# Performance work log

Measured on AMD Instinct MI355X. Metric: run time of the kernel, lower is better.

Reference implementation:

```python
import jax, jax.numpy as jnp
import numpy as np

X_DIM, XC_DIM, G_DIM = 45, 10, 20
P_DIM = XC_DIM * G_DIM  # 200
N_ITER, KAPPA, LAMDA, YITA = 5, 0.8, 0.9999, 0.5
B = 131072


def _mlp(h, W1, b1, W2, b2):
    # MLP(in,out) with activation=(elu, None): elu hidden, linear out
    return jax.nn.elu(h @ W1 + b1) @ W2 + b2


def _f_p(h):
    # hippocampal nonlinearity: leaky_relu clamped to [-1, 1]
    return jnp.clip(jax.nn.leaky_relu(h), -1.0, 1.0)


def _retrieve(q, M0):
    # iterative Hopfield-like attractor retrieval (n_iteration fixed, small)
    p = q
    for _ in range(N_ITER):
        p = _f_p(KAPPA * p + p @ M0)
    return p


def setup_inputs() -> dict:
    key = jax.random.key(0)
    ks = jax.random.split(key, 12)
    s = 0.1  # small param scale for numerical sanity
    return {
        "x": jax.random.normal(ks[0], (B, X_DIM), jnp.float32),
        "g": jax.random.normal(ks[1], (B, G_DIM), jnp.float32),
        # M buffer starts at zeros in the module; use small noise so retrieval is nontrivial
        "M": 0.01 * jax.random.normal(ks[2], (1, P_DIM, P_DIM), jnp.float32),
        "W_comp": s * jax.random.normal(ks[3], (X_DIM, XC_DIM), jnp.float32),
        "W1_ie": s * jax.random.normal(ks[4], (G_DIM, 2 * G_DIM), jnp.float32),
        "b1_ie": jnp.zeros((2 * G_DIM,), jnp.float32),
        "W2_ie": s * jax.random.normal(ks[5], (2 * G_DIM, G_DIM), jnp.float32),
        "b2_ie": jnp.zeros((G_DIM,), jnp.float32),
        "W1_gg": s * jax.random.normal(ks[6], (G_DIM, 2 * G_DIM), jnp.float32),
        "b1_gg": jnp.zeros((2 * G_DIM,), jnp.float32),
        "W2_gg": s * jax.random.normal(ks[7], (2 * G_DIM, G_DIM), jnp.float32),
        "b2_gg": jnp.zeros((G_DIM,), jnp.float32),
        "W_sp": s * jax.random.normal(ks[8], (XC_DIM, X_DIM), jnp.float32),
        "b_sp": jnp.zeros((X_DIM,), jnp.float32),
    }


def reference(x, g, M, W_comp, W1_ie, b1_ie, W2_ie, b2_ie,
              W1_gg, b1_gg, W2_gg, b2_gg, W_sp, b_sp):
    # fixed structural matrices (buffers in torch)
    W_tile = jnp.kron(jnp.ones((1, G_DIM), jnp.float32), jnp.eye(XC_DIM, dtype=jnp.float32))   # [xc, p]
    W_repeat = jnp.kron(jnp.eye(G_DIM, dtype=jnp.float32), jnp.ones((1, XC_DIM), jnp.float32))  # [g, p]
    M0 = M[0]

    # compress sensory -> hippocampal sensory component
    xc = x @ W_comp                 # [B, xc]
    x_ = xc @ W_tile                # [B, p]

    # retrieve from memory with sensory cue, infer entorhinal g
    px = _retrieve(x_, M0)          # [B, p]
    g_inf = jnp.clip(_mlp(px @ W_repeat.T, W1_ie, b1_ie, W2_ie, b2_ie), -1.0, 1.0)  # [B, g]

    # path integration / entorhinal transition, project to hippocampus
    g2 = jnp.tanh(_mlp(g, W1_gg, b1_gg, W2_gg, b2_gg))  # [B, g]
    g_ = g2 @ W_repeat              # [B, p]

    # retrieve with entorhinal cue, predict sensory observation
    p = _retrieve(g_, M0)           # [B, p]
    x_inf = (p @ W_tile.T) @ W_sp + b_sp  # [B, x]

    # inferred hippocampal state (conjunction) and Hebbian memory update
    p_inf = _f_p(g_ * x_)           # [B, p]
    hebb = ((p_inf - p).T @ (p_inf + p)) / jnp.asarray(x.shape[0], x.dtype)  # [p, p]
    M_new = LAMDA * M + YITA * hebb[None]

    return (g_inf, x_inf, g_, x_, M_new)
```

## Files before the change

### kernel.cpp

```cpp
#include <hip/hip_runtime.h>

#define B_TOTAL 131072
#define PD 200
#define KAPPA 0.8f
#define LAMDA 0.9999f
#define YITA 0.5f
#define MS_KS 216
#define HB_RS 72

typedef short short8 __attribute__((ext_vector_type(8)));
typedef short short4v __attribute__((ext_vector_type(4)));
typedef float f32x16 __attribute__((ext_vector_type(16)));
typedef unsigned uint4v __attribute__((ext_vector_type(4)));

static __device__ __forceinline__ float bf2f(unsigned short h) {
  union { unsigned u; float f; } v; v.u = ((unsigned)h) << 16; return v.f;
}
static __device__ __forceinline__ unsigned short f2bf(float f) {
  union { float f; unsigned u; } v; v.f = f;
  unsigned r = v.u + 0x7FFFu + ((v.u >> 16) & 1u);
  return (unsigned short)(r >> 16);
}
static __device__ __forceinline__ float fp_nl(float v) {
  float t = fmaxf(v, 0.01f * v);
  return fminf(1.f, fmaxf(-1.f, t));
}
static __device__ __forceinline__ unsigned pkbf(float lo, float hi) {
  unsigned r;
  asm("v_cvt_pk_bf16_f32 %0, %1, %2" : "=v"(r) : "v"(lo), "v"(hi));
  return r;
}
static __device__ __forceinline__ void swap32(unsigned &a, unsigned &b) {
  asm("s_nop 1\n\tv_permlane32_swap_b32 %0, %1" : "+v"(a), "+v"(b));
}
static __device__ __forceinline__ uint4v mk4(unsigned a, unsigned b, unsigned c, unsigned d) {
  uint4v v; v[0] = a; v[1] = b; v[2] = c; v[3] = d; return v;
}
static __device__ __forceinline__ short8 u4s8(uint4v w) {
  union { uint4v u; short8 s; } x; x.u = w; return x.s;
}

__global__ void tem_init_m(const float* __restrict__ Min, float* __restrict__ oM) {
  int i = blockIdx.x * 256 + threadIdx.x;
  if (i < PD * PD) oM[i] = LAMDA * Min[i];
}

__global__ __launch_bounds__(256, 4) void tem_pre(
    const float* __restrict__ xin, const float* __restrict__ gin,
    const float* __restrict__ Wc,
    const float* __restrict__ W1gg, const float* __restrict__ b1gg,
    const float* __restrict__ W2gg, const float* __restrict__ b2gg,
    float* __restrict__ o_g, float* __restrict__ o_x) {
  __shared__ unsigned short xcS[128 * 10];
  __shared__ float g2S[128 * 20];
  const int tid = threadIdx.x;
  const int r0 = blockIdx.x * 128;

  if (tid < 128) {
    const int rq = r0 + tid;
    float gv[20];
#pragma unroll
    for (int i = 0; i < 20; ++i) gv[i] = gin[(size_t)rq * 20 + i];
    float out20[20];
#pragma unroll
    for (int o = 0; o < 20; ++o) out20[o] = b2gg[o];
#pragma unroll 1
    for (int u = 0; u < 40; ++u) {
      float hu = b1gg[u];
#pragma unroll
      for (int i = 0; i < 20; ++i) hu += gv[i] * W1gg[i * 40 + u];
      hu = (hu > 0.f) ? hu : (expf(hu) - 1.f);
#pragma unroll
      for (int o = 0; o < 20; ++o) out20[o] += hu * W2gg[u * 20 + o];
    }
#pragma unroll
    for (int o = 0; o < 20; ++o) g2S[tid * 20 + o] = tanhf(out20[o]);
  } else {
    const int rr2 = tid - 128;
    const int rq = r0 + rr2;
    float xc[10];
#pragma unroll
    for (int o = 0; o < 10; ++o) xc[o] = 0.f;
#pragma unroll 1
    for (int j = 0; j < 45; ++j) {
      const float xv = xin[(size_t)rq * 45 + j];
#pragma unroll
      for (int o = 0; o < 10; ++o) xc[o] += xv * Wc[j * 10 + o];
    }
#pragma unroll
    for (int o = 0; o < 10; ++o) xcS[rr2 * 10 + o] = f2bf(xc[o]);
  }
  __syncthreads();
  for (int i = tid; i < 128 * 200; i += 256) {
    const int rP = i / 200, j = i - rP * 200;
    o_g[(size_t)(r0 + rP) * 200 + j] = g2S[rP * 20 + j / 10];
    o_x[(size_t)(r0 + rP) * 200 + j] = bf2f(xcS[rP * 10 + (j % 10)]);
  }
}

#define LDMS(nt, kc) (*(const short8*)(Ms + (((nt) * 32 + cl) * MS_KS + (kc) * 16 + hi * 8)))
#define MFMA_AG(ACC, A, B) asm("v_mfma_f32_32x32x16_bf16 %0, %1, %2, %0" : "+a"(ACC) : "v"(A), "v"(B))

#define STEP(PF, KC) do { \
  const short8 _b = u4s8(PF); \
  { const short8 _a = LDMS(0, KC); MFMA_AG(acc0, _a, _b); } \
  { const short8 _a = LDMS(1, KC); MFMA_AG(acc1, _a, _b); } \
  { const short8 _a = LDMS(2, KC); MFMA_AG(acc2, _a, _b); } \
  { const short8 _a = LDMS(3, KC); MFMA_AG(acc3, _a, _b); } \
  { const short8 _a = LDMS(4, KC); MFMA_AG(acc4, _a, _b); } \
  { const short8 _a = LDMS(5, KC); MFMA_AG(acc5, _a, _b); } \
  { const short8 _a = LDMS(6, KC); MFMA_AG(acc6, _a, _b); } \
  __builtin_amdgcn_sched_barrier(0); \
} while (0)

#define REPACK_LO(ACC, PF) do { \
  unsigned P0 = pkbf(fp_nl(ACC[0]), fp_nl(ACC[1])); \
  unsigned P1 = pkbf(fp_nl(ACC[2]), fp_nl(ACC[3])); \
  unsigned P2 = pkbf(fp_nl(ACC[4]), fp_nl(ACC[5])); \
  unsigned P3 = pkbf(fp_nl(ACC[6]), fp_nl(ACC[7])); \
  swap32(P0, P2); swap32(P1, P3); \
  PF = mk4(P0, P1, P2, P3); \
} while (0)
#define REPACK_HI(ACC, PF) do { \
  unsigned P4 = pkbf(fp_nl(ACC[8]),  fp_nl(ACC[9])); \
  unsigned P5 = pkbf(fp_nl(ACC[10]), fp_nl(ACC[11])); \
  unsigned P6 = pkbf(fp_nl(ACC[12]), fp_nl(ACC[13])); \
  unsigned P7 = pkbf(fp_nl(ACC[14]), fp_nl(ACC[15])); \
  swap32(P4, P6); swap32(P5, P7); \
  PF = mk4(P4, P5, P6, P7); \
} while (0)

#define ITER5 do { \
  f32x16 acc0 = {}, acc1 = {}, acc2 = {}, acc3 = {}, acc4 = {}, acc5 = {}, acc6 = {}; \
  STEP(pfA0, 0);  STEP(pfA1, 1);  STEP(pfA2, 2);  STEP(pfA3, 3); \
  STEP(pfA4, 4);  STEP(pfA5, 5);  STEP(pfA6, 6);  STEP(pfA7, 7); \
  STEP(pfA8, 8);  STEP(pfA9, 9);  STEP(pfA10, 10); STEP(pfA11, 11); \
  STEP(pfA12, 12); \
  REPACK_LO(acc0, pfA0);  REPACK_HI(acc0, pfA1); \
  REPACK_LO(acc1, pfA2);  REPACK_HI(acc1, pfA3); \
  REPACK_LO(acc2, pfA4);  REPACK_HI(acc2, pfA5); \
  REPACK_LO(acc3, pfA6);  REPACK_HI(acc3, pfA7); \
  REPACK_LO(acc4, pfA8);  REPACK_HI(acc4, pfA9); \
  REPACK_LO(acc5, pfA10); REPACK_HI(acc5, pfA11); \
  REPACK_LO(acc6, pfA12); \
} while (0)

#define FORR_LO(M_) M_(pfA0,0) M_(pfA1,16) M_(pfA2,32) M_(pfA3,48) M_(pfA4,64) M_(pfA5,80) \
                    M_(pfA6,96) M_(pfA7,112) M_(pfA8,128) M_(pfA9,144) M_(pfA10,160) M_(pfA11,176) M_(pfA12,192)
#define FORR_HI(M_) M_(pfA0,8) M_(pfA1,24) M_(pfA2,40) M_(pfA3,56) M_(pfA4,72) M_(pfA5,88) \
                    M_(pfA6,104) M_(pfA7,120) M_(pfA8,136) M_(pfA9,152) M_(pfA10,168) M_(pfA11,184)

#define INX(PF, BB) PF = mk4( \
  pkbf(xcv[((BB) + 0) % 10], xcv[((BB) + 1) % 10]), \
  pkbf(xcv[((BB) + 2) % 10], xcv[((BB) + 3) % 10]), \
  pkbf(xcv[((BB) + 4) % 10], xcv[((BB) + 5) % 10]), \
  pkbf(xcv[((BB) + 6) % 10], xcv[((BB) + 7) % 10]));
#define ING(PF, BB) PF = mk4( \
  pkbf(g2v[((BB) + 0) / 10], g2v[((BB) + 1) / 10]), \
  pkbf(g2v[((BB) + 2) / 10], g2v[((BB) + 3) / 10]), \
  pkbf(g2v[((BB) + 4) / 10], g2v[((BB) + 5) / 10]), \
  pkbf(g2v[((BB) + 6) / 10], g2v[((BB) + 7) / 10]));

#define E1W(W, F) { bins[(F) / 10] += bf2f((unsigned short)((W) & 0xFFFFu)); \
                    bins[((F) + 1) / 10] += bf2f((unsigned short)((W) >> 16)); }
#define E1PF(PF, BB) { E1W(PF[0], (BB) + 0) E1W(PF[1], (BB) + 2) E1W(PF[2], (BB) + 4) E1W(PF[3], (BB) + 6) }

#define E2AW(W, F) { ta[(F) % 10] += bf2f((unsigned short)((W) & 0xFFFFu)); \
                     ta[((F) + 1) % 10] += bf2f((unsigned short)((W) >> 16)); }
#define E2APF(PF, BB) { E2AW(PF[0], (BB) + 0) E2AW(PF[1], (BB) + 2) E2AW(PF[2], (BB) + 4) E2AW(PF[3], (BB) + 6) }

#define STG(PF, SL) (((uint4v*)Stg)[(wid * 4 + (SL)) * 64 + lane] = PF)

__global__ __launch_bounds__(512, 1) void tem_main(
    const float* __restrict__ xin, const float* __restrict__ gin,
    const float* __restrict__ Min, const float* __restrict__ Wc,
    const float* __restrict__ W1ie, const float* __restrict__ b1ie,
    const float* __restrict__ W2ie, const float* __restrict__ b2ie,
    const float* __restrict__ W1gg, const float* __restrict__ b1gg,
    const float* __restrict__ W2gg, const float* __restrict__ b2gg,
    const float* __restrict__ Wsp, const float* __restrict__ bsp,
    float* __restrict__ o_ginf, float* __restrict__ o_xinf,
    unsigned short* __restrict__ dWp, unsigned short* __restrict__ sWp) {
  __shared__ __attribute__((aligned(16))) unsigned short Ms[224 * MS_KS];
  __shared__ unsigned short xcS[256 * 10];
  __shared__ float g2S[256 * 20];
  __shared__ __attribute__((aligned(16))) unsigned Stg[8 * 4 * 64 * 4];

  const int tid = threadIdx.x;
  const int lane = tid & 63;
  const int wid = tid >> 6;
  const int cl = lane & 31;
  const int hi = lane >> 5;
  const int r0 = blockIdx.x * 256;

  {
    unsigned* Ms32 = (unsigned*)Ms;
    for (int i = tid; i < 224 * MS_KS / 2; i += 512) Ms32[i] = 0u;
  }
  __syncthreads();
  for (int i = tid; i < 200 * 224; i += 512) {
    const int k = i / 224, n = i - k * 224;
    if (n < 200) {
      float v = Min[k * 200 + n];
      if (k == n) v += KAPPA;
      Ms[n * MS_KS + k] = f2bf(v);
    }
  }

  if (tid < 256) {
    const int rq = r0 + tid;
    float gv[20];
#pragma unroll
    for (int i = 0; i < 20; ++i) gv[i] = gin[(size_t)rq * 20 + i];
    float h[40];
#pragma unroll
    for (int u = 0; u < 40; ++u) h[u] = b1gg[u];
#pragma unroll
    for (int i = 0; i < 20; ++i)
#pragma unroll
      for (int u = 0; u < 40; ++u) h[u] += gv[i] * W1gg[i * 40 + u];
#pragma unroll
    for (int u = 0; u < 40; ++u) h[u] = (h[u] > 0.f) ? h[u] : (expf(h[u]) - 1.f);
#pragma unroll
    for (int o = 0; o < 20; ++o) {
      float v = b2gg[o];
#pragma unroll
      for (int u = 0; u < 40; ++u) v += h[u] * W2gg[u * 20 + o];
      g2S[tid * 20 + o] = tanhf(v);
    }
  } else {
    const int rr2 = tid - 256;
    const int rq = r0 + rr2;
    float xc[10];
#pragma unroll
    for (int o = 0; o < 10; ++o) xc[o] = 0.f;
#pragma unroll 1
    for (int j = 0; j < 45; ++j) {
      const float xv = xin[(size_t)rq * 45 + j];
#pragma unroll
      for (int o = 0; o < 10; ++o) xc[o] += xv * Wc[j * 10 + o];
    }
#pragma unroll
    for (int o = 0; o < 10; ++o) xcS[rr2 * 10 + o] = f2bf(xc[o]);
  }
  __syncthreads();

  const int rr = wid * 32 + cl;
  const int r = r0 + rr;

  uint4v pfA0, pfA1, pfA2, pfA3, pfA4, pfA5, pfA6, pfA7, pfA8, pfA9, pfA10, pfA11, pfA12;

  {
    float xcv[10];
#pragma unroll
    for (int o = 0; o < 10; ++o) xcv[o] = bf2f(xcS[rr * 10 + o]);
    if (hi == 0) { FORR_LO(INX) }
    else         { FORR_HI(INX) pfA12 = mk4(0u, 0u, 0u, 0u); }
  }
#pragma unroll 1
  for (int it = 0; it < 5; ++it) { ITER5; }
  {
    float bins[20];
#pragma unroll
    for (int t = 0; t < 20; ++t) bins[t] = 0.f;
    if (hi == 0) { FORR_LO(E1PF) } else { FORR_HI(E1PF) }
#pragma unroll
    for (int t = 0; t < 20; ++t) bins[t] += __shfl_xor(bins[t], 32);
    float h[40];
#pragma unroll
    for (int u = 0; u < 40; ++u) h[u] = b1ie[u];
#pragma unroll
    for (int gg = 0; gg < 20; ++gg) {
      const float bv = bins[gg];
#pragma unroll
      for (int u = 0; u < 40; ++u) h[u] += bv * W1ie[gg * 40 + u];
    }
#pragma unroll
    for (int u = 0; u < 40; ++u) h[u] = (h[u] > 0.f) ? h[u] : (expf(h[u]) - 1.f);
#pragma unroll
    for (int oi = 0; oi < 10; ++oi) {
      const int o = hi * 10 + oi;
      float v = b2ie[o];
#pragma unroll
      for (int u = 0; u < 40; ++u) v += h[u] * W2ie[u * 20 + o];
      o_ginf[(size_t)r * 20 + o] = fminf(1.f, fmaxf(-1.f, v));
    }
  }

  {
    float g2v[20];
#pragma unroll
    for (int o = 0; o < 20; ++o) g2v[o] = g2S[rr * 20 + o];
    if (hi == 0) { FORR_LO(ING) }
    else         { FORR_HI(ING) pfA12 = mk4(0u, 0u, 0u, 0u); }
  }
#pragma unroll 1
  for (int it = 0; it < 5; ++it) { ITER5; }
  {
    float ta[10];
#pragma unroll
    for (int t = 0; t < 10; ++t) ta[t] = 0.f;
    if (hi == 0) { FORR_LO(E2APF) } else { FORR_HI(E2APF) }
#pragma unroll
    for (int t = 0; t < 10; ++t) ta[t] += __shfl_xor(ta[t], 32);
    const int o0 = hi ? 23 : 0, o1 = hi ? 45 : 23;
#pragma unroll 1
    for (int o = o0; o < o1; ++o) {
      float v = bsp[o];
#pragma unroll
      for (int a = 0; a < 10; ++a) v += ta[a] * Wsp[a * 45 + o];
      o_xinf[(size_t)r * 45 + o] = v;
    }
  }
  {
    unsigned int* dW32 = (unsigned int*)dWp;
    unsigned int* sW32 = (unsigned int*)sWp;
#pragma unroll 1
    for (int rnd = 0; rnd < 4; ++rnd) {
      if (rnd == 0)      { STG(pfA0, 0);  STG(pfA1, 1);  STG(pfA2, 2);   STG(pfA3, 3);  }
      else if (rnd == 1) { STG(pfA4, 0);  STG(pfA5, 1);  STG(pfA6, 2);   STG(pfA7, 3);  }
      else if (rnd == 2) { STG(pfA8, 0);  STG(pfA9, 1);  STG(pfA10, 2);  STG(pfA11, 3); }
      else               { STG(pfA12, 0); }
      asm volatile("s_waitcnt lgkmcnt(0)" ::: "memory");
      __builtin_amdgcn_sched_barrier(0);
      const int nIt = (rnd == 3) ? 2 : 16;
#pragma unroll 1
      for (int itw = 0; itw < nIt; ++itw) {
        const int idx = itw * 64 + lane;
        const int row = idx >> 5;
        const int jpo = idx & 31;
        const int jp = rnd * 32 + jpo;
        if (jp < 100) {
          const int kcl = jpo >> 3, rem = jpo & 7;
          const int hi2 = rem >> 2, jw = rem & 3;
          const unsigned word = Stg[(((wid * 4 + kcl) * 2 + hi2) * 32 + row) * 4 + jw];
          const int rB = wid * 32 + row;
          const int j0 = jp * 2;
          const float p0 = bf2f((unsigned short)(word & 0xFFFFu));
          const float p1 = bf2f((unsigned short)(word >> 16));
          const float x0 = bf2f(xcS[rB * 10 + (j0 % 10)]);
          const float x1 = bf2f(xcS[rB * 10 + ((j0 + 1) % 10)]);
          const float pi0 = fp_nl(g2S[rB * 20 + (j0 / 10)] * x0);
          const float pi1 = fp_nl(g2S[rB * 20 + ((j0 + 1) / 10)] * x1);
          const unsigned dpack = (unsigned)f2bf(pi0 - p0) | ((unsigned)f2bf(pi1 - p1) << 16);
          const unsigned spack = (unsigned)f2bf(pi0 + p0) | ((unsigned)f2bf(pi1 + p1) << 16);
          const size_t oidx = (size_t)(r0 + rB) * 100 + jp;
          dW32[oidx] = dpack;
          sW32[oidx] = spack;
        }
      }
      __builtin_amdgcn_sched_barrier(0);
    }
  }
}

__global__ __launch_bounds__(448, 1) void tem_hebb(
    const unsigned short* __restrict__ dWp, const unsigned short* __restrict__ sWp,
    float* __restrict__ oM) {
  __shared__ __attribute__((aligned(16))) unsigned short dT[224 * HB_RS];
  __shared__ __attribute__((aligned(16))) unsigned short sT[224 * HB_RS];
  const int tid = threadIdx.x;
  const int lane = tid & 63, wid = tid >> 6;
  const int cl = lane & 31, hi = lane >> 5;
  for (int i = tid; i < 224 * HB_RS; i += 448) { dT[i] = 0; sT[i] = 0; }
  f32x16 hacc[7];
#pragma unroll
  for (int nt = 0; nt < 7; ++nt)
#pragma unroll
    for (int q = 0; q < 16; ++q) hacc[nt][q] = 0.f;
  const int kbase = blockIdx.x * 512;
#pragma unroll 1
  for (int sub = 0; sub < 8; ++sub) {
    __syncthreads();
    const int kb = kbase + sub * 64;
#pragma unroll 1
    for (int i = tid; i < 64 * 50; i += 448) {
      const int rr = i / 50, fq = i - rr * 50;
      const int f0 = fq * 4;
      const short4v d4 = *(const short4v*)(dWp + ((size_t)(kb + rr) * 200 + f0));
      const short4v s4 = *(const short4v*)(sWp + ((size_t)(kb + rr) * 200 + f0));
#pragma unroll
      for (int q = 0; q < 4; ++q) {
        dT[(f0 + q) * HB_RS + rr] = (unsigned short)d4[q];
        sT[(f0 + q) * HB_RS + rr] = (unsigned short)s4[q];
      }
    }
    __syncthreads();
#pragma unroll
    for (int kc = 0; kc < 4; ++kc) {
      const short8 af = *(const short8*)(dT + ((wid * 32 + cl) * HB_RS + kc * 16 + hi * 8));
#pragma unroll
      for (int nt = 0; nt < 7; ++nt) {
        const short8 bfr = *(const short8*)(sT + ((nt * 32 + cl) * HB_RS + kc * 16 + hi * 8));
        hacc[nt] = __builtin_amdgcn_mfma_f32_32x32x16_bf16(af, bfr, hacc[nt], 0, 0, 0);
      }
    }
  }
  const float scale = YITA / (float)B_TOTAL;
#pragma unroll
  for (int nt = 0; nt < 7; ++nt) {
    const int j = nt * 32 + cl;
    if (j < 200) {
#pragma unroll
      for (int rg = 0; rg < 16; ++rg) {
        const int ii = wid * 32 + (rg & 3) + 8 * (rg >> 2) + 4 * hi;
        if (ii < 200) atomicAdd(&oM[ii * 200 + j], hacc[nt][rg] * scale);
      }
    }
  }
}

extern "C" void kernel_launch(void* const* d_in, const int* in_sizes, int n_in,
                              void* d_out, int out_size, void* d_ws, size_t ws_size,
                              hipStream_t stream) {
  (void)in_sizes; (void)n_in; (void)out_size; (void)ws_size;
  const float* xin  = (const float*)d_in[0];
  const float* gin  = (const float*)d_in[1];
  const float* Min  = (const float*)d_in[2];
  const float* Wc   = (const float*)d_in[3];
  const float* W1ie = (const float*)d_in[4];
  const float* b1ie = (const float*)d_in[5];
  const float* W2ie = (const float*)d_in[6];
  const float* b2ie = (const float*)d_in[7];
  const float* W1gg = (const float*)d_in[8];
  const float* b1gg = (const float*)d_in[9];
  const float* W2gg = (const float*)d_in[10];
  const float* b2gg = (const float*)d_in[11];
  const float* Wsp  = (const float*)d_in[12];
  const float* bsp  = (const float*)d_in[13];

  float* out = (float*)d_out;
  float* o_ginf = out;
  float* o_xinf = out + (size_t)B_TOTAL * 20;
  float* o_g    = out + (size_t)B_TOTAL * 65;
  float* o_x    = out + (size_t)B_TOTAL * 265;
  float* o_M    = out + (size_t)B_TOTAL * 465;

  unsigned short* dWp = (unsigned short*)d_ws;
  unsigned short* sWp = dWp + (size_t)B_TOTAL * PD;

  tem_init_m<<<(PD * PD + 255) / 256, 256, 0, stream>>>(Min, o_M);
  tem_pre<<<1024, 256, 0, stream>>>(xin, gin, Wc, W1gg, b1gg, W2gg, b2gg, o_g, o_x);
  tem_main<<<512, 512, 0, stream>>>(xin, gin, Min, Wc, W1ie, b1ie, W2ie, b2ie,
                                    W1gg, b1gg, W2gg, b2gg, Wsp, bsp,
                                    o_ginf, o_xinf, dWp, sWp);
  tem_hebb<<<256, 448, 0, stream>>>(dWp, sWp, o_M);
}
```

Measured before the change: 495.2 us.

## Store Hebbian workspace feature-major and stage per-row outputs through LDS

The d/s workspace is now written feature-major ([200][B]) rather than row-major, so the Hebbian kernel can load MFMA fragments straight from global memory without the LDS transpose and its two barriers per sub-chunk. The g_inf and x_inf outputs are also staged in shared memory and written back coalesced rather than as strided per-row stores. The trade-offs are extra block-wide syncs in the main kernel, only 2 of 8 waves writing the workspace, and unstaged global loads in the Hebbian kernel that reuse the A fragment less.

```diff
diff --git a/kernel.cpp b/kernel.cpp
--- a/kernel.cpp
+++ b/kernel.cpp
@@ -6,10 +6,8 @@
 #define LAMDA 0.9999f
 #define YITA 0.5f
 #define MS_KS 216
-#define HB_RS 72
 
 typedef short short8 __attribute__((ext_vector_type(8)));
-typedef short short4v __attribute__((ext_vector_type(4)));
 typedef float f32x16 __attribute__((ext_vector_type(16)));
 typedef unsigned uint4v __attribute__((ext_vector_type(4)));
 
@@ -169,7 +167,7 @@
                      ta[((F) + 1) % 10] += bf2f((unsigned short)((W) >> 16)); }
 #define E2APF(PF, BB) { E2AW(PF[0], (BB) + 0) E2AW(PF[1], (BB) + 2) E2AW(PF[2], (BB) + 4) E2AW(PF[3], (BB) + 6) }
 
-#define STG(PF, SL) (((uint4v*)Stg)[(wid * 4 + (SL)) * 64 + lane] = PF)
+#define STG(PF, SL) (((uint4v*)StgRaw)[(wid * 4 + (SL)) * 64 + lane] = PF)
 
 __global__ __launch_bounds__(512, 1) void tem_main(
     const float* __restrict__ xin, const float* __restrict__ gin,
@@ -184,7 +182,10 @@
   __shared__ __attribute__((aligned(16))) unsigned short Ms[224 * MS_KS];
   __shared__ unsigned short xcS[256 * 10];
   __shared__ float g2S[256 * 20];
-  __shared__ __attribute__((aligned(16))) unsigned Stg[8 * 4 * 64 * 4];
+  __shared__ __attribute__((aligned(16))) char StgRaw[32768];
+
+  unsigned* StgU = (unsigned*)StgRaw;
+  float* StgF = (float*)StgRaw;
 
   const int tid = threadIdx.x;
   const int lane = tid & 63;
@@ -283,9 +284,12 @@
       float v = b2ie[o];
 #pragma unroll
       for (int u = 0; u < 40; ++u) v += h[u] * W2ie[u * 20 + o];
-      o_ginf[(size_t)r * 20 + o] = fminf(1.f, fmaxf(-1.f, v));
-    }
-  }
+      StgF[rr * 20 + o] = fminf(1.f, fmaxf(-1.f, v));
+    }
+  }
+  __syncthreads();
+  for (int i = tid; i < 256 * 20; i += 512) o_ginf[(size_t)r0 * 20 + i] = StgF[i];
+  __syncthreads();
 
   {
     float g2v[20];
@@ -303,13 +307,23 @@
     if (hi == 0) { FORR_LO(E2APF) } else { FORR_HI(E2APF) }
 #pragma unroll
     for (int t = 0; t < 10; ++t) ta[t] += __shfl_xor(ta[t], 32);
-    const int o0 = hi ? 23 : 0, o1 = hi ? 45 : 23;
-#pragma unroll 1
-    for (int o = o0; o < o1; ++o) {
-      float v = bsp[o];
-#pragma unroll
-      for (int a = 0; a < 10; ++a) v += ta[a] * Wsp[a * 45 + o];
-      o_xinf[(size_t)r * 45 + o] = v;
+#pragma unroll 1
+    for (int ph = 0; ph < 2; ++ph) {
+      if ((rr >> 7) == ph) {
+        const int rL = rr & 127;
+        const int o0 = hi ? 23 : 0, o1 = hi ? 45 : 23;
+#pragma unroll 1
+        for (int o = o0; o < o1; ++o) {
+          float v = bsp[o];
+#pragma unroll
+          for (int a = 0; a < 10; ++a) v += ta[a] * Wsp[a * 45 + o];
+          StgF[rL * 45 + o] = v;
+        }
+      }
+      __syncthreads();
+      for (int i = tid; i < 128 * 45; i += 512)
+        o_xinf[((size_t)r0 + ph * 128) * 45 + i] = StgF[i];
+      __syncthreads();
     }
   }
   {
@@ -321,35 +335,29 @@
       else if (rnd == 1) { STG(pfA4, 0);  STG(pfA5, 1);  STG(pfA6, 2);   STG(pfA7, 3);  }
       else if (rnd == 2) { STG(pfA8, 0);  STG(pfA9, 1);  STG(pfA10, 2);  STG(pfA11, 3); }
       else               { STG(pfA12, 0); }
-      asm volatile("s_waitcnt lgkmcnt(0)" ::: "memory");
-      __builtin_amdgcn_sched_barrier(0);
-      const int nIt = (rnd == 3) ? 2 : 16;
-#pragma unroll 1
-      for (int itw = 0; itw < nIt; ++itw) {
-        const int idx = itw * 64 + lane;
-        const int row = idx >> 5;
-        const int jpo = idx & 31;
-        const int jp = rnd * 32 + jpo;
-        if (jp < 100) {
-          const int kcl = jpo >> 3, rem = jpo & 7;
-          const int hi2 = rem >> 2, jw = rem & 3;
-          const unsigned word = Stg[(((wid * 4 + kcl) * 2 + hi2) * 32 + row) * 4 + jw];
-          const int rB = wid * 32 + row;
-          const int j0 = jp * 2;
-          const float p0 = bf2f((unsigned short)(word & 0xFFFFu));
-          const float p1 = bf2f((unsigned short)(word >> 16));
-          const float x0 = bf2f(xcS[rB * 10 + (j0 % 10)]);
-          const float x1 = bf2f(xcS[rB * 10 + ((j0 + 1) % 10)]);
-          const float pi0 = fp_nl(g2S[rB * 20 + (j0 / 10)] * x0);
-          const float pi1 = fp_nl(g2S[rB * 20 + ((j0 + 1) / 10)] * x1);
-          const unsigned dpack = (unsigned)f2bf(pi0 - p0) | ((unsigned)f2bf(pi1 - p1) << 16);
-          const unsigned spack = (unsigned)f2bf(pi0 + p0) | ((unsigned)f2bf(pi1 + p1) << 16);
-          const size_t oidx = (size_t)(r0 + rB) * 100 + jp;
-          dW32[oidx] = dpack;
-          sW32[oidx] = spack;
+      __syncthreads();
+      if (wid < 2) {
+        const int base = wid * 128;
+        const int ra = base + 2 * lane;
+        const int rb = ra + 1;
+        const int nF = (rnd == 3) ? 8 : 64;
+#pragma unroll 1
+        for (int f = 0; f < nF; ++f) {
+          const int fo = rnd * 64 + f;
+          const int kcl = f >> 4, hi2 = (f >> 3) & 1, jw = (f >> 1) & 3, hf = f & 1;
+          const unsigned wa = StgU[(((ra >> 5) * 4 + kcl) * 64 + hi2 * 32 + (ra & 31)) * 4 + jw];
+          const unsigned wb = StgU[(((rb >> 5) * 4 + kcl) * 64 + hi2 * 32 + (rb & 31)) * 4 + jw];
+          const float p0 = bf2f((unsigned short)(hf ? (wa >> 16) : (wa & 0xFFFFu)));
+          const float p1 = bf2f((unsigned short)(hf ? (wb >> 16) : (wb & 0xFFFFu)));
+          const int fg = fo / 10, fx = fo - fg * 10;
+          const float pi0 = fp_nl(g2S[ra * 20 + fg] * bf2f(xcS[ra * 10 + fx]));
+          const float pi1 = fp_nl(g2S[rb * 20 + fg] * bf2f(xcS[rb * 10 + fx]));
+          const size_t oidx = (size_t)fo * (B_TOTAL / 2) + (size_t)(r0 + base) / 2 + lane;
+          dW32[oidx] = (unsigned)f2bf(pi0 - p0) | ((unsigned)f2bf(pi1 - p1) << 16);
+          sW32[oidx] = (unsigned)f2bf(pi0 + p0) | ((unsigned)f2bf(pi1 + p1) << 16);
         }
       }
-      __builtin_amdgcn_sched_barrier(0);
+      __syncthreads();
     }
   }
 }
@@ -357,43 +365,31 @@
 __global__ __launch_bounds__(448, 1) void tem_hebb(
     const unsigned short* __restrict__ dWp, const unsigned short* __restrict__ sWp,
     float* __restrict__ oM) {
-  __shared__ __attribute__((aligned(16))) unsigned short dT[224 * HB_RS];
-  __shared__ __attribute__((aligned(16))) unsigned short sT[224 * HB_RS];
   const int tid = threadIdx.x;
   const int lane = tid & 63, wid = tid >> 6;
   const int cl = lane & 31, hi = lane >> 5;
-  for (int i = tid; i < 224 * HB_RS; i += 448) { dT[i] = 0; sT[i] = 0; }
   f32x16 hacc[7];
 #pragma unroll
   for (int nt = 0; nt < 7; ++nt)
 #pragma unroll
     for (int q = 0; q < 16; ++q) hacc[nt][q] = 0.f;
-  const int kbase = blockIdx.x * 512;
-#pragma unroll 1
-  for (int sub = 0; sub < 8; ++sub) {
-    __syncthreads();
-    const int kb = kbase + sub * 64;
-#pragma unroll 1
-    for (int i = tid; i < 64 * 50; i += 448) {
-      const int rr = i / 50, fq = i - rr * 50;
-      const int f0 = fq * 4;
-      const short4v d4 = *(const short4v*)(dWp + ((size_t)(kb + rr) * 200 + f0));
-      const short4v s4 = *(const short4v*)(sWp + ((size_t)(kb + rr) * 200 + f0));
-#pragma unroll
-      for (int q = 0; q < 4; ++q) {
-        dT[(f0 + q) * HB_RS + rr] = (unsigned short)d4[q];
-        sT[(f0 + q) * HB_RS + rr] = (unsigned short)s4[q];
-      }
-    }
-    __syncthreads();
-#pragma unroll
-    for (int kc = 0; kc < 4; ++kc) {
-      const short8 af = *(const short8*)(dT + ((wid * 32 + cl) * HB_RS + kc * 16 + hi * 8));
-#pragma unroll
-      for (int nt = 0; nt < 7; ++nt) {
-        const short8 bfr = *(const short8*)(sT + ((nt * 32 + cl) * HB_RS + kc * 16 + hi * 8));
-        hacc[nt] = __builtin_amdgcn_mfma_f32_32x32x16_bf16(af, bfr, hacc[nt], 0, 0, 0);
-      }
+
+  const int fa = wid * 32 + cl;
+  const size_t arow = (size_t)fa * B_TOTAL;
+  const int kb0 = blockIdx.x * 512;
+  const short8 zf = {0, 0, 0, 0, 0, 0, 0, 0};
+
+#pragma unroll 1
+  for (int kch = 0; kch < 32; ++kch) {
+    const int kb = kb0 + kch * 16 + hi * 8;
+    short8 a = zf;
+    if (fa < 200) a = *(const short8*)(dWp + arow + kb);
+#pragma unroll
+    for (int nt = 0; nt < 7; ++nt) {
+      const int fb = nt * 32 + cl;
+      short8 b = zf;
+      if (fb < 200) b = *(const short8*)(sWp + (size_t)fb * B_TOTAL + kb);
+      hacc[nt] = __builtin_amdgcn_mfma_f32_32x32x16_bf16(a, b, hacc[nt], 0, 0, 0);
     }
   }
   const float scale = YITA / (float)B_TOTAL;
@@ -437,7 +433,7 @@
   float* o_M    = out + (size_t)B_TOTAL * 465;
 
   unsigned short* dWp = (unsigned short*)d_ws;
-  unsigned short* sWp = dWp + (size_t)B_TOTAL * PD;
+  unsigned short* sWp = dWp + (size_t)PD * B_TOTAL;
 
   tem_init_m<<<(PD * PD + 255) / 256, 256, 0, stream>>>(Min, o_M);
   tem_pre<<<1024, 256, 0, stream>>>(xin, gin, Wc, W1gg, b1gg, W2gg, b2gg, o_g, o_x);
```

Measured after the change: 547.4 us. +10.5%, slower.
